# Kernel tuning notes

Measured on AMD Instinct MI355X. Metric: run time of the kernel, lower is better.

Reference implementation:

```python
import jax, jax.numpy as jnp
import numpy as np

N_EMBD = 1024
N_HEAD = 16
HEAD_DIM = N_EMBD // N_HEAD


def setup_inputs() -> dict:
    key = jax.random.key(0)
    ks = jax.random.split(key, 5)
    x = jax.random.normal(ks[0], (2, 2048, N_EMBD), dtype=jnp.float32)
    # Linear params, scaled like torch default init (~U(-1/sqrt(fan_in),..)) approximated with small normal
    s = 1.0 / np.sqrt(N_EMBD)
    W_qkv = jax.random.normal(ks[1], (N_EMBD, 3 * N_EMBD), dtype=jnp.float32) * s
    b_qkv = jax.random.normal(ks[2], (3 * N_EMBD,), dtype=jnp.float32) * s
    W_proj = jax.random.normal(ks[3], (N_EMBD, N_EMBD), dtype=jnp.float32) * s
    b_proj = jax.random.normal(ks[4], (N_EMBD,), dtype=jnp.float32) * s
    return {"x": x, "W_qkv": W_qkv, "b_qkv": b_qkv, "W_proj": W_proj, "b_proj": b_proj}


def reference(x, W_qkv, b_qkv, W_proj, b_proj):
    B, T, C = x.shape
    qkv = x @ W_qkv + b_qkv                              # [B,T,3C]
    qkv = qkv.reshape(B, T, 3, N_HEAD, HEAD_DIM)
    qkv = jnp.transpose(qkv, (2, 0, 3, 1, 4))            # [3,B,H,T,D]
    q, k, v = qkv[0], qkv[1], qkv[2]
    scale = HEAD_DIM ** -0.5
    att = jnp.einsum('bhqd,bhkd->bhqk', q, k) * scale    # [B,H,T,T]
    causal = jnp.tril(jnp.ones((T, T), dtype=bool))
    att = jnp.where(causal, att, -jnp.inf)
    att = jax.nn.softmax(att, axis=-1)
    y = jnp.einsum('bhqk,bhkd->bhqd', att, v)            # [B,H,T,D]
    y = jnp.transpose(y, (0, 2, 1, 3)).reshape(B, T, C)
    return y @ W_proj + b_proj
```

## Files before the change

kernel.cpp:

```cpp
#include <hip/hip_runtime.h>
#include <hip/hip_bf16.h>
#include <stdint.h>

#define N_EMBD 1024
#define N_HEAD 16
#define HEAD_DIM 64
#define T_SEQ 2048
#define BATCH 2
#define M_TOK (BATCH * T_SEQ)

typedef short bf16x8 __attribute__((ext_vector_type(8)));
typedef float f32x4 __attribute__((ext_vector_type(4)));

__device__ __forceinline__ void gload_lds16(const void* g, void* l) {
  __builtin_amdgcn_global_load_lds(
      (const __attribute__((address_space(1))) void*)g,
      (__attribute__((address_space(3))) void*)l, 16, 0, 0);
}

__device__ __forceinline__ uint16_t f2bf(float x) {
  uint32_t u = __float_as_uint(x);
  uint32_t r = (u + 0x7FFFu + ((u >> 16) & 1u)) >> 16;
  return (uint16_t)r;
}

__global__ void convert_f32_bf16(const float* __restrict__ in,
                                 uint16_t* __restrict__ out, int n) {
  int i = (blockIdx.x * blockDim.x + threadIdx.x) * 4;
  int stride = gridDim.x * blockDim.x * 4;
  for (; i + 3 < n; i += stride) {
    float4 v = *(const float4*)(in + i);
    ushort4 o;
    o.x = f2bf(v.x); o.y = f2bf(v.y); o.z = f2bf(v.z); o.w = f2bf(v.w);
    *(ushort4*)(out + i) = o;
  }
}

__global__ void transpose_convert(const float* __restrict__ W,
                                  uint16_t* __restrict__ Wt, int R, int C_) {
  __shared__ uint16_t t[64][65];
  int c0 = blockIdx.x * 64, r0 = blockIdx.y * 64;
  int lc = threadIdx.x & 63, lr4 = threadIdx.x >> 6;
#pragma unroll
  for (int rr = 0; rr < 16; ++rr) {
    int r = rr * 4 + lr4;
    t[r][lc] = f2bf(W[(size_t)(r0 + r) * C_ + c0 + lc]);
  }
  __syncthreads();
#pragma unroll
  for (int rr = 0; rr < 16; ++rr) {
    int r = rr * 4 + lr4;
    Wt[(size_t)(c0 + r) * R + r0 + lc] = t[lc][r];
  }
}

__global__ void transpose_v(const uint16_t* __restrict__ qkv,
                            uint16_t* __restrict__ Vt) {
  __shared__ uint16_t t[64][65];
  int t0 = blockIdx.x * 64;
  int bh = blockIdx.y;
  int b = bh >> 4, h = bh & 15;
  int lc = threadIdx.x & 63, lr4 = threadIdx.x >> 6;
  const uint16_t* src =
      qkv + (size_t)(b * T_SEQ) * (3 * N_EMBD) + 2 * N_EMBD + h * 64;
#pragma unroll
  for (int rr = 0; rr < 16; ++rr) {
    int r = rr * 4 + lr4;
    t[r][lc] = src[(size_t)(t0 + r) * (3 * N_EMBD) + lc];
  }
  __syncthreads();
  uint16_t* dst = Vt + (size_t)bh * 64 * T_SEQ;
#pragma unroll
  for (int rr = 0; rr < 16; ++rr) {
    int d = rr * 4 + lr4;
    dst[(size_t)d * T_SEQ + t0 + lc] = t[lc][d];
  }
}

template <int OUT_BF16>
__global__ __launch_bounds__(256) void gemm_bt(
    const uint16_t* __restrict__ A, const uint16_t* __restrict__ Bt,
    const float* __restrict__ bias, void* __restrict__ Cv, int M, int N,
    int K) {
  __shared__ __attribute__((aligned(16))) uint16_t sA[2][128 * 32];
  __shared__ __attribute__((aligned(16))) uint16_t sB[2][128 * 32];
  int tid = threadIdx.x;
  int w = tid >> 6, l = tid & 63;
  int wm = w >> 1, wn = w & 1;
  int ql = l & 15, hi = l >> 4;
  size_t m0 = (size_t)blockIdx.x * 128, n0 = (size_t)blockIdx.y * 128;
  f32x4 acc[4][4] = {};

#pragma unroll
  for (int r = 0; r < 2; ++r) {
    int base = r * 256 + (w << 6);
    int idx = base + l;
    gload_lds16(A + (m0 + (idx >> 2)) * K + (idx & 3) * 8, &sA[0][0] + base * 8);
    gload_lds16(Bt + (n0 + (idx >> 2)) * K + (idx & 3) * 8, &sB[0][0] + base * 8);
  }

  int cur = 0;
  for (int kt = 0; kt < K; kt += 32) {
    if (kt + 32 < K) {
#pragma unroll
      for (int r = 0; r < 2; ++r) {
        int base = r * 256 + (w << 6);
        int idx = base + l;
        gload_lds16(A + (m0 + (idx >> 2)) * K + kt + 32 + (idx & 3) * 8,
                    &sA[cur ^ 1][0] + base * 8);
        gload_lds16(Bt + (n0 + (idx >> 2)) * K + kt + 32 + (idx & 3) * 8,
                    &sB[cur ^ 1][0] + base * 8);
      }
      asm volatile("s_waitcnt vmcnt(4)" ::: "memory");
    } else {
      asm volatile("s_waitcnt vmcnt(0)" ::: "memory");
    }
    __builtin_amdgcn_s_barrier();
    __builtin_amdgcn_sched_barrier(0);
    bf16x8 af[4], bfr[4];
#pragma unroll
    for (int i = 0; i < 4; i++)
      af[i] = *(const bf16x8*)(&sA[cur][0] + (wm * 64 + i * 16 + ql) * 32 + hi * 8);
#pragma unroll
    for (int j = 0; j < 4; j++)
      bfr[j] = *(const bf16x8*)(&sB[cur][0] + (wn * 64 + j * 16 + ql) * 32 + hi * 8);
#pragma unroll
    for (int i = 0; i < 4; i++)
#pragma unroll
      for (int j = 0; j < 4; j++)
        acc[i][j] = __builtin_amdgcn_mfma_f32_16x16x32_bf16(af[i], bfr[j],
                                                            acc[i][j], 0, 0, 0);
    __builtin_amdgcn_sched_barrier(0);
    __builtin_amdgcn_s_barrier();
    cur ^= 1;
  }

#pragma unroll
  for (int i = 0; i < 4; i++) {
    size_t m = m0 + wm * 64 + i * 16 + hi * 4;
#pragma unroll
    for (int j = 0; j < 4; j++) {
      size_t n = n0 + wn * 64 + j * 16 + ql;
      float bv = bias[n];
#pragma unroll
      for (int r = 0; r < 4; r++) {
        float v = acc[i][j][r] + bv;
        if (OUT_BF16)
          ((uint16_t*)Cv)[(m + r) * N + n] = f2bf(v);
        else
          ((float*)Cv)[(m + r) * N + n] = v;
      }
    }
  }
}

__device__ __forceinline__ void sm_pack(const f32x4* sfr, f32x4* acc,
                                        float& m_run, float& l_part, bool mask,
                                        int qloc, int hi, bool lo, int sl0,
                                        int sl1, bf16x8& pf0o, bf16x8& pf1o) {
  float sv[16];
  if (mask) {
    const int kb0 = 4 * hi;
#pragma unroll
    for (int f = 0; f < 4; ++f)
#pragma unroll
      for (int r = 0; r < 4; ++r)
        sv[4 * f + r] = (16 * f + kb0 + r <= qloc) ? sfr[f][r] : -1e30f;
  } else {
#pragma unroll
    for (int f = 0; f < 4; ++f)
#pragma unroll
      for (int r = 0; r < 4; ++r) sv[4 * f + r] = sfr[f][r];
  }
  float x0 = fmaxf(fmaxf(sv[0], sv[1]), fmaxf(sv[2], sv[3]));
  float x1 = fmaxf(fmaxf(sv[4], sv[5]), fmaxf(sv[6], sv[7]));
  float x2 = fmaxf(fmaxf(sv[8], sv[9]), fmaxf(sv[10], sv[11]));
  float x3 = fmaxf(fmaxf(sv[12], sv[13]), fmaxf(sv[14], sv[15]));
  float tmax = fmaxf(fmaxf(x0, x1), fmaxf(x2, x3));
  if (__any(tmax > m_run)) {
    float tm = fmaxf(tmax, __shfl_xor(tmax, 16));
    tm = fmaxf(tm, __shfl_xor(tm, 32));
    float m_new = fmaxf(m_run, tm);
    float corr = __expf(m_run - m_new);
    m_run = m_new;
    l_part *= corr;
#pragma unroll
    for (int d = 0; d < 4; ++d) acc[d] *= corr;
  }
  float pv[16];
#pragma unroll
  for (int i2 = 0; i2 < 16; ++i2) pv[i2] = __expf(sv[i2] - m_run);
  float s01 = (pv[0] + pv[1]) + (pv[2] + pv[3]);
  float s23 = (pv[4] + pv[5]) + (pv[6] + pv[7]);
  float s45 = (pv[8] + pv[9]) + (pv[10] + pv[11]);
  float s67 = (pv[12] + pv[13]) + (pv[14] + pv[15]);
  l_part += (s01 + s23) + (s45 + s67);
  uint32_t wp[8];
#pragma unroll
  for (int f = 0; f < 4; ++f) {
    asm("v_cvt_pk_bf16_f32 %0, %1, %2"
        : "=v"(wp[2 * f]) : "v"(pv[4 * f]), "v"(pv[4 * f + 1]));
    asm("v_cvt_pk_bf16_f32 %0, %1, %2"
        : "=v"(wp[2 * f + 1]) : "v"(pv[4 * f + 2]), "v"(pv[4 * f + 3]));
  }
  union { uint32_t u[4]; bf16x8 v; } pf0, pf1;
  {
    uint32_t a0 = __shfl((int)wp[0], sl0), b0 = __shfl((int)wp[2], sl0);
    uint32_t a1 = __shfl((int)wp[1], sl0), b1 = __shfl((int)wp[3], sl0);
    uint32_t a2 = __shfl((int)wp[0], sl1), b2 = __shfl((int)wp[2], sl1);
    uint32_t a3 = __shfl((int)wp[1], sl1), b3 = __shfl((int)wp[3], sl1);
    pf0.u[0] = lo ? a0 : b0; pf0.u[1] = lo ? a1 : b1;
    pf0.u[2] = lo ? a2 : b2; pf0.u[3] = lo ? a3 : b3;
  }
  {
    uint32_t a0 = __shfl((int)wp[4], sl0), b0 = __shfl((int)wp[6], sl0);
    uint32_t a1 = __shfl((int)wp[5], sl0), b1 = __shfl((int)wp[7], sl0);
    uint32_t a2 = __shfl((int)wp[4], sl1), b2 = __shfl((int)wp[6], sl1);
    uint32_t a3 = __shfl((int)wp[5], sl1), b3 = __shfl((int)wp[7], sl1);
    pf1.u[0] = lo ? a0 : b0; pf1.u[1] = lo ? a1 : b1;
    pf1.u[2] = lo ? a2 : b2; pf1.u[3] = lo ? a3 : b3;
  }
  pf0o = pf0.v;
  pf1o = pf1.v;
}

__device__ __forceinline__ void load_q_scaled(const uint16_t* Qb, int qg,
                                              int hi, bf16x8& q0, bf16x8& q1) {
  const size_t rs = 3 * N_EMBD;
  q0 = *(const bf16x8*)(Qb + (size_t)qg * rs + hi * 8);
  q1 = *(const bf16x8*)(Qb + (size_t)qg * rs + 32 + hi * 8);
#pragma unroll
  for (int j = 0; j < 8; ++j) {
    uint16_t u = (uint16_t)q0[j];
    q0[j] = (short)(((u & 0x7f80u) >= 0x180u) ? (u - 0x180u) : (u & 0x8000u));
    uint16_t v = (uint16_t)q1[j];
    q1[j] = (short)(((v & 0x7f80u) >= 0x180u) ? (v - 0x180u) : (v & 0x8000u));
  }
}

__device__ __forceinline__ void write_o(const f32x4* acc, float l_part,
                                        uint16_t* y, int b, int h, int qg,
                                        int hi) {
  float lt = l_part + __shfl_xor(l_part, 16);
  lt += __shfl_xor(lt, 32);
  float inv = 1.0f / lt;
  uint16_t* yrow = y + (size_t)(b * T_SEQ + qg) * N_EMBD + h * 64;
#pragma unroll
  for (int d = 0; d < 4; ++d) {
    uint32_t o01, o23;
    float v0 = acc[d][0] * inv, v1 = acc[d][1] * inv;
    float v2 = acc[d][2] * inv, v3 = acc[d][3] * inv;
    asm("v_cvt_pk_bf16_f32 %0, %1, %2" : "=v"(o01) : "v"(v0), "v"(v1));
    asm("v_cvt_pk_bf16_f32 %0, %1, %2" : "=v"(o23) : "v"(v2), "v"(v3));
    *(uint32_t*)(yrow + d * 16 + hi * 4) = o01;
    *(uint32_t*)(yrow + d * 16 + hi * 4 + 2) = o23;
  }
}

__global__ __launch_bounds__(128, 2) void attn_kernel(
    const uint16_t* __restrict__ qkv, const uint16_t* __restrict__ Vt,
    uint16_t* __restrict__ y) {
  __shared__ __attribute__((aligned(16))) uint16_t sK[2][64 * 64];
  __shared__ __attribute__((aligned(16))) uint16_t sV[2][64 * 64];

  int tid = threadIdx.x;
  int w = tid >> 6, l = tid & 63;
  int ql = l & 15, hi = l >> 4;
  int id = blockIdx.x;
  int xcd = id & 7;
  int bh = xcd * 4 + ((id >> 3) & 3);
  int qt = 31 - (id >> 5);
  int b = bh >> 4, h = bh & 15;
  const size_t rs = 3 * N_EMBD;
  const uint16_t* Qb = qkv + (size_t)(b * T_SEQ) * rs + h * 64;
  const uint16_t* Kb = Qb + N_EMBD;
  const uint16_t* Vb = Vt + (size_t)bh * 64 * T_SEQ;
  const bool lo = hi < 2;
  const int sl0 = ql + ((hi & 1) << 5);
  const int sl1 = sl0 + 16;
  const int qlocA = w * 16 + ql;
  const int qlocB = qlocA + 32;
  const int qgA = qt * 64 + qlocA;
  const int qgB = qt * 64 + qlocB;

  bf16x8 qfA0, qfA1, qfB0, qfB1;
  load_q_scaled(Qb, qgA, hi, qfA0, qfA1);
  load_q_scaled(Qb, qgB, hi, qfB0, qfB1);

  f32x4 accA[4] = {}, accB[4] = {};
  float mA = -1e30f, lA = 0.f, mB = -1e30f, lB = 0.f;
  const int xr = (ql & 7) * 8;
  const int nIter = qt + 1;

#pragma unroll
  for (int s2 = 0; s2 < 4; ++s2) {
    int base16 = s2 * 128 + w * 64;
    int idx = base16 + l;
    int row = idx >> 3, c = idx & 7;
    int d8 = c ^ (row & 7);
    gload_lds16(Kb + (size_t)row * rs + d8 * 8, &sK[0][0] + base16 * 8);
    gload_lds16(Vb + (size_t)row * T_SEQ + d8 * 8, &sV[0][0] + base16 * 8);
  }

  int cur = 0;
  for (int t = 0; t < nIter; ++t) {
    if (t + 1 < nIter) {
      const int kvn = (t + 1) << 6;
#pragma unroll
      for (int s2 = 0; s2 < 4; ++s2) {
        int base16 = s2 * 128 + w * 64;
        int idx = base16 + l;
        int row = idx >> 3, c = idx & 7;
        int d8 = c ^ (row & 7);
        gload_lds16(Kb + (size_t)(kvn + row) * rs + d8 * 8,
                    &sK[cur ^ 1][0] + base16 * 8);
        gload_lds16(Vb + (size_t)row * T_SEQ + kvn + d8 * 8,
                    &sV[cur ^ 1][0] + base16 * 8);
      }
      asm volatile("s_waitcnt vmcnt(8)" ::: "memory");
    } else {
      asm volatile("s_waitcnt vmcnt(0)" ::: "memory");
    }
    __builtin_amdgcn_s_barrier();
    __builtin_amdgcn_sched_barrier(0);
    const uint16_t* kb_l = &sK[cur][0];
    const uint16_t* vb_l = &sV[cur][0];
    bf16x8 kf[8];
#pragma unroll
    for (int f = 0; f < 4; ++f) {
      kf[2 * f] = *(const bf16x8*)(kb_l + (16 * f + ql) * 64 + ((hi * 8) ^ xr));
      kf[2 * f + 1] =
          *(const bf16x8*)(kb_l + (16 * f + ql) * 64 + (((4 + hi) * 8) ^ xr));
    }
    f32x4 sA[4] = {}, sB[4] = {};
    __builtin_amdgcn_s_setprio(1);
#pragma unroll
    for (int f = 0; f < 4; ++f) {
      sA[f] = __builtin_amdgcn_mfma_f32_16x16x32_bf16(kf[2 * f], qfA0, sA[f], 0, 0, 0);
      sA[f] = __builtin_amdgcn_mfma_f32_16x16x32_bf16(kf[2 * f + 1], qfA1, sA[f], 0, 0, 0);
      sB[f] = __builtin_amdgcn_mfma_f32_16x16x32_bf16(kf[2 * f], qfB0, sB[f], 0, 0, 0);
      sB[f] = __builtin_amdgcn_mfma_f32_16x16x32_bf16(kf[2 * f + 1], qfB1, sB[f], 0, 0, 0);
    }
    __builtin_amdgcn_s_setprio(0);
    bf16x8 vf[8];
#pragma unroll
    for (int d = 0; d < 4; ++d) {
      vf[2 * d] = *(const bf16x8*)(vb_l + (16 * d + ql) * 64 + ((hi * 8) ^ xr));
      vf[2 * d + 1] =
          *(const bf16x8*)(vb_l + (16 * d + ql) * 64 + (((4 + hi) * 8) ^ xr));
    }
    bf16x8 pA0, pA1, pB0, pB1;
    sm_pack(sA, accA, mA, lA, t == qt, qlocA, hi, lo, sl0, sl1, pA0, pA1);
    sm_pack(sB, accB, mB, lB, t == qt, qlocB, hi, lo, sl0, sl1, pB0, pB1);
    __builtin_amdgcn_s_setprio(1);
#pragma unroll
    for (int d = 0; d < 4; ++d) {
      accA[d] = __builtin_amdgcn_mfma_f32_16x16x32_bf16(vf[2 * d], pA0, accA[d], 0, 0, 0);
      accA[d] = __builtin_amdgcn_mfma_f32_16x16x32_bf16(vf[2 * d + 1], pA1, accA[d], 0, 0, 0);
      accB[d] = __builtin_amdgcn_mfma_f32_16x16x32_bf16(vf[2 * d], pB0, accB[d], 0, 0, 0);
      accB[d] = __builtin_amdgcn_mfma_f32_16x16x32_bf16(vf[2 * d + 1], pB1, accB[d], 0, 0, 0);
    }
    __builtin_amdgcn_s_setprio(0);
    __builtin_amdgcn_sched_barrier(0);
    __builtin_amdgcn_s_barrier();
    cur ^= 1;
  }

  write_o(accA, lA, y, b, h, qgA, hi);
  write_o(accB, lB, y, b, h, qgB, hi);
}

extern "C" void kernel_launch(void* const* d_in, const int* in_sizes, int n_in,
                              void* d_out, int out_size, void* d_ws,
                              size_t ws_size, hipStream_t stream) {
  const float* x = (const float*)d_in[0];
  const float* Wqkv = (const float*)d_in[1];
  const float* bqkv = (const float*)d_in[2];
  const float* Wproj = (const float*)d_in[3];
  const float* bproj = (const float*)d_in[4];
  float* out = (float*)d_out;

  uint8_t* ws = (uint8_t*)d_ws;
  uint16_t* xb = (uint16_t*)(ws);
  uint16_t* wqkvT = (uint16_t*)(ws + (8u << 20));
  uint16_t* wprojT = (uint16_t*)(ws + (14u << 20));
  uint16_t* qkv = (uint16_t*)(ws + (16u << 20));
  uint16_t* vt = (uint16_t*)(ws + (40u << 20));
  uint16_t* yb = (uint16_t*)(ws + (48u << 20));

  convert_f32_bf16<<<dim3(4096), dim3(256), 0, stream>>>(x, xb,
                                                         M_TOK * N_EMBD);
  transpose_convert<<<dim3(3072 / 64, 1024 / 64), dim3(256), 0, stream>>>(
      Wqkv, wqkvT, 1024, 3072);
  transpose_convert<<<dim3(1024 / 64, 1024 / 64), dim3(256), 0, stream>>>(
      Wproj, wprojT, 1024, 1024);
  gemm_bt<1><<<dim3(M_TOK / 128, 3072 / 128), dim3(256), 0, stream>>>(
      xb, wqkvT, bqkv, qkv, M_TOK, 3072, 1024);
  transpose_v<<<dim3(T_SEQ / 64, 32), dim3(256), 0, stream>>>(qkv, vt);
  attn_kernel<<<dim3(1024), dim3(128), 0, stream>>>(qkv, vt, yb);
  gemm_bt<0><<<dim3(M_TOK / 128, 1024 / 128), dim3(256), 0, stream>>>(
      yb, wprojT, bproj, out, M_TOK, 1024, 1024);
}
```

Measured before the change: 135.4 us.

## Halve attention query tile per block and load V directly from global

Each attention block now handles 32 query rows instead of 64, so the grid doubles to 2048 blocks and occupancy is raised to 4 blocks per SM. V fragments are read straight from global memory into registers rather than staged through LDS, which removes the V shared buffer and its async copies. The intent is better load balance and latency hiding for the causal triangle. In exchange, each K tile is loaded and shared across fewer queries, so K traffic rises, and the V global reads are uncoalesced and sit on the critical path.

```diff
diff --git a/kernel.cpp b/kernel.cpp
--- a/kernel.cpp
+++ b/kernel.cpp
@@ -156,7 +156,7 @@
 
 __device__ __forceinline__ void sm_pack(const f32x4* sfr, f32x4* acc,
                                         float& m_run, float& l_part, bool mask,
-                                        int qloc, int hi, bool lo, int sl0,
+                                        int qthr, int hi, bool lo, int sl0,
                                         int sl1, bf16x8& pf0o, bf16x8& pf1o) {
   float sv[16];
   if (mask) {
@@ -165,7 +165,7 @@
     for (int f = 0; f < 4; ++f)
 #pragma unroll
       for (int r = 0; r < 4; ++r)
-        sv[4 * f + r] = (16 * f + kb0 + r <= qloc) ? sfr[f][r] : -1e30f;
+        sv[4 * f + r] = (16 * f + kb0 + r <= qthr) ? sfr[f][r] : -1e30f;
   } else {
 #pragma unroll
     for (int f = 0; f < 4; ++f)
@@ -257,11 +257,10 @@
   }
 }
 
-__global__ __launch_bounds__(128, 2) void attn_kernel(
+__global__ __launch_bounds__(128, 4) void attn_kernel(
     const uint16_t* __restrict__ qkv, const uint16_t* __restrict__ Vt,
     uint16_t* __restrict__ y) {
   __shared__ __attribute__((aligned(16))) uint16_t sK[2][64 * 64];
-  __shared__ __attribute__((aligned(16))) uint16_t sV[2][64 * 64];
 
   int tid = threadIdx.x;
   int w = tid >> 6, l = tid & 63;
@@ -269,7 +268,7 @@
   int id = blockIdx.x;
   int xcd = id & 7;
   int bh = xcd * 4 + ((id >> 3) & 3);
-  int qt = 31 - (id >> 5);
+  int s = 63 - (id >> 5);
   int b = bh >> 4, h = bh & 15;
   const size_t rs = 3 * N_EMBD;
   const uint16_t* Qb = qkv + (size_t)(b * T_SEQ) * rs + h * 64;
@@ -278,19 +277,17 @@
   const bool lo = hi < 2;
   const int sl0 = ql + ((hi & 1) << 5);
   const int sl1 = sl0 + 16;
-  const int qlocA = w * 16 + ql;
-  const int qlocB = qlocA + 32;
-  const int qgA = qt * 64 + qlocA;
-  const int qgB = qt * 64 + qlocB;
-
-  bf16x8 qfA0, qfA1, qfB0, qfB1;
-  load_q_scaled(Qb, qgA, hi, qfA0, qfA1);
-  load_q_scaled(Qb, qgB, hi, qfB0, qfB1);
-
-  f32x4 accA[4] = {}, accB[4] = {};
-  float mA = -1e30f, lA = 0.f, mB = -1e30f, lB = 0.f;
+  const int qg = s * 32 + w * 16 + ql;
+  const int nIter = (s + 2) >> 1;
+  const int qthr = qg - ((nIter - 1) << 6);
+
+  bf16x8 qf0, qf1;
+  load_q_scaled(Qb, qg, hi, qf0, qf1);
+
+  f32x4 acc[4] = {};
+  float m_run = -1e30f, l_part = 0.f;
   const int xr = (ql & 7) * 8;
-  const int nIter = qt + 1;
+  const uint16_t* vptr = Vb + (size_t)ql * T_SEQ + hi * 8;
 
 #pragma unroll
   for (int s2 = 0; s2 < 4; ++s2) {
@@ -299,13 +296,20 @@
     int row = idx >> 3, c = idx & 7;
     int d8 = c ^ (row & 7);
     gload_lds16(Kb + (size_t)row * rs + d8 * 8, &sK[0][0] + base16 * 8);
-    gload_lds16(Vb + (size_t)row * T_SEQ + d8 * 8, &sV[0][0] + base16 * 8);
   }
 
   int cur = 0;
   for (int t = 0; t < nIter; ++t) {
+    const int kv0 = t << 6;
+    bf16x8 vf[8];
+#pragma unroll
+    for (int d = 0; d < 4; ++d) {
+      vf[2 * d] = *(const bf16x8*)(vptr + (size_t)(16 * d) * T_SEQ + kv0);
+      vf[2 * d + 1] =
+          *(const bf16x8*)(vptr + (size_t)(16 * d) * T_SEQ + kv0 + 32);
+    }
     if (t + 1 < nIter) {
-      const int kvn = (t + 1) << 6;
+      const int kvn = kv0 + 64;
 #pragma unroll
       for (int s2 = 0; s2 < 4; ++s2) {
         int base16 = s2 * 128 + w * 64;
@@ -314,17 +318,14 @@
         int d8 = c ^ (row & 7);
         gload_lds16(Kb + (size_t)(kvn + row) * rs + d8 * 8,
                     &sK[cur ^ 1][0] + base16 * 8);
-        gload_lds16(Vb + (size_t)row * T_SEQ + kvn + d8 * 8,
-                    &sV[cur ^ 1][0] + base16 * 8);
       }
+      asm volatile("s_waitcnt vmcnt(12)" ::: "memory");
+    } else {
       asm volatile("s_waitcnt vmcnt(8)" ::: "memory");
-    } else {
-      asm volatile("s_waitcnt vmcnt(0)" ::: "memory");
     }
     __builtin_amdgcn_s_barrier();
     __builtin_amdgcn_sched_barrier(0);
     const uint16_t* kb_l = &sK[cur][0];
-    const uint16_t* vb_l = &sV[cur][0];
     bf16x8 kf[8];
 #pragma unroll
     for (int f = 0; f < 4; ++f) {
@@ -332,33 +333,24 @@
       kf[2 * f + 1] =
           *(const bf16x8*)(kb_l + (16 * f + ql) * 64 + (((4 + hi) * 8) ^ xr));
     }
-    f32x4 sA[4] = {}, sB[4] = {};
+    f32x4 sfr[4] = {};
     __builtin_amdgcn_s_setprio(1);
 #pragma unroll
     for (int f = 0; f < 4; ++f) {
-      sA[f] = __builtin_amdgcn_mfma_f32_16x16x32_bf16(kf[2 * f], qfA0, sA[f], 0, 0, 0);
-      sA[f] = __builtin_amdgcn_mfma_f32_16x16x32_bf16(kf[2 * f + 1], qfA1, sA[f], 0, 0, 0);
-      sB[f] = __builtin_amdgcn_mfma_f32_16x16x32_bf16(kf[2 * f], qfB0, sB[f], 0, 0, 0);
-      sB[f] = __builtin_amdgcn_mfma_f32_16x16x32_bf16(kf[2 * f + 1], qfB1, sB[f], 0, 0, 0);
+      sfr[f] = __builtin_amdgcn_mfma_f32_16x16x32_bf16(kf[2 * f], qf0, sfr[f], 0, 0, 0);
+      sfr[f] =
+          __builtin_amdgcn_mfma_f32_16x16x32_bf16(kf[2 * f + 1], qf1, sfr[f], 0, 0, 0);
     }
     __builtin_amdgcn_s_setprio(0);
-    bf16x8 vf[8];
+    bf16x8 p0, p1;
+    sm_pack(sfr, acc, m_run, l_part, t == nIter - 1, qthr, hi, lo, sl0, sl1,
+            p0, p1);
+    __builtin_amdgcn_s_setprio(1);
 #pragma unroll
     for (int d = 0; d < 4; ++d) {
-      vf[2 * d] = *(const bf16x8*)(vb_l + (16 * d + ql) * 64 + ((hi * 8) ^ xr));
-      vf[2 * d + 1] =
-          *(const bf16x8*)(vb_l + (16 * d + ql) * 64 + (((4 + hi) * 8) ^ xr));
-    }
-    bf16x8 pA0, pA1, pB0, pB1;
-    sm_pack(sA, accA, mA, lA, t == qt, qlocA, hi, lo, sl0, sl1, pA0, pA1);
-    sm_pack(sB, accB, mB, lB, t == qt, qlocB, hi, lo, sl0, sl1, pB0, pB1);
-    __builtin_amdgcn_s_setprio(1);
-#pragma unroll
-    for (int d = 0; d < 4; ++d) {
-      accA[d] = __builtin_amdgcn_mfma_f32_16x16x32_bf16(vf[2 * d], pA0, accA[d], 0, 0, 0);
-      accA[d] = __builtin_amdgcn_mfma_f32_16x16x32_bf16(vf[2 * d + 1], pA1, accA[d], 0, 0, 0);
-      accB[d] = __builtin_amdgcn_mfma_f32_16x16x32_bf16(vf[2 * d], pB0, accB[d], 0, 0, 0);
-      accB[d] = __builtin_amdgcn_mfma_f32_16x16x32_bf16(vf[2 * d + 1], pB1, accB[d], 0, 0, 0);
+      acc[d] = __builtin_amdgcn_mfma_f32_16x16x32_bf16(vf[2 * d], p0, acc[d], 0, 0, 0);
+      acc[d] =
+          __builtin_amdgcn_mfma_f32_16x16x32_bf16(vf[2 * d + 1], p1, acc[d], 0, 0, 0);
     }
     __builtin_amdgcn_s_setprio(0);
     __builtin_amdgcn_sched_barrier(0);
@@ -366,8 +358,7 @@
     cur ^= 1;
   }
 
-  write_o(accA, lA, y, b, h, qgA, hi);
-  write_o(accB, lB, y, b, h, qgB, hi);
+  write_o(acc, l_part, y, b, h, qg, hi);
 }
 
 extern "C" void kernel_launch(void* const* d_in, const int* in_sizes, int n_in,
@@ -397,7 +388,7 @@
   gemm_bt<1><<<dim3(M_TOK / 128, 3072 / 128), dim3(256), 0, stream>>>(
       xb, wqkvT, bqkv, qkv, M_TOK, 3072, 1024);
   transpose_v<<<dim3(T_SEQ / 64, 32), dim3(256), 0, stream>>>(qkv, vt);
-  attn_kernel<<<dim3(1024), dim3(128), 0, stream>>>(qkv, vt, yb);
+  attn_kernel<<<dim3(2048), dim3(128), 0, stream>>>(qkv, vt, yb);
   gemm_bt<0><<<dim3(M_TOK / 128, 1024 / 128), dim3(256), 0, stream>>>(
       yb, wprojT, bproj, out, M_TOK, 1024, 1024);
 }
```

Measured after the change: 155.9 us. +15.1%, slower.
